# Kernel optimization log

Hardware: AMD Instinct MI355X
Metric: run time of the kernel (lower is better)

The kernel has to match this reference:

```python
import jax, jax.numpy as jnp
import numpy as np

N, E = 50000, 800000
IN_C, OUT_C, HEADS = 128, 16, 8
EDGE_DIM = 1
NEG_SLOPE = 0.2
LN_EPS = 1e-5


def setup_inputs() -> dict:
    key = jax.random.key(0)
    ks = jax.random.split(key, 12)
    s = 1.0 / np.sqrt(IN_C)
    HC = OUT_C * HEADS
    return {
        "x": jax.random.normal(ks[0], (N, IN_C), jnp.float32),
        "edge_index": jax.random.randint(ks[1], (2, E), 0, N, jnp.int32),
        "edge_attr": jax.random.normal(ks[2], (E, EDGE_DIM), jnp.float32),
        "W": jax.random.normal(ks[3], (IN_C, HC), jnp.float32) * s,
        "b": jnp.zeros((HC,), jnp.float32),
        "att_src": jax.random.normal(ks[4], (HEADS, OUT_C), jnp.float32) * s,
        "att_dst": jax.random.normal(ks[5], (HEADS, OUT_C), jnp.float32) * s,
        "att_edge": jax.random.normal(ks[6], (HEADS, OUT_C), jnp.float32) * s,
        "lin_edge_w": jax.random.normal(ks[7], (EDGE_DIM, HC), jnp.float32) * s,
        "lin_edge_b": jnp.zeros((HC,), jnp.float32),
        "gamma": jnp.ones((HC,), jnp.float32),
        "beta": jnp.zeros((HC,), jnp.float32),
    }


def _segment_softmax(logits, seg, num_segments):
    # numerically-stable softmax over edges grouped by destination node
    m = jax.ops.segment_max(logits, seg, num_segments=num_segments)
    ex = jnp.exp(logits - m[seg])
    z = jax.ops.segment_sum(ex, seg, num_segments=num_segments)
    return ex / (z[seg] + 1e-16)


def reference(x, edge_index, edge_attr, W, b, att_src, att_dst, att_edge,
              lin_edge_w, lin_edge_b, gamma, beta):
    n = x.shape[0]
    src, dst = edge_index[0], edge_index[1]
    # GAT conv: per-head transform, edge-indexed attention, segment softmax, scatter-add
    h = (x @ W).reshape(n, HEADS, OUT_C)                      # [N,H,C]
    a_src = jnp.einsum('nhc,hc->nh', h, att_src)              # [N,H]
    a_dst = jnp.einsum('nhc,hc->nh', h, att_dst)
    e = (edge_attr @ lin_edge_w + lin_edge_b).reshape(-1, HEADS, OUT_C)
    a_edge = jnp.einsum('ehc,hc->eh', e, att_edge)            # [E,H]
    logits = jax.nn.leaky_relu(a_src[src] + a_dst[dst] + a_edge, NEG_SLOPE)
    alpha = _segment_softmax(logits, dst, n)                  # [E,H]
    msg = alpha[..., None] * h[src]                           # [E,H,C]
    out = jax.ops.segment_sum(msg, dst, num_segments=n).reshape(n, -1) + b
    # residual (in_channels == heads*out_channels -> identity projection)
    out = out + x
    # LayerNorm + ELU (dropout is eval-mode identity)
    mu = jnp.mean(out, axis=-1, keepdims=True)
    var = jnp.var(out, axis=-1, keepdims=True)
    out = (out - mu) * jax.lax.rsqrt(var + LN_EPS) * gamma + beta
    return jax.nn.elu(out)
```

## Files before the change

kernel.cpp:

```cpp
#include <hip/hip_runtime.h>
#include <hip/hip_bf16.h>

#define N_NODES 50000
#define N_EDGES 800000
#define IN_C 128
#define HC 128
#define HEADS 8
#define NEG_SLOPE 0.2f
#define LN_EPS 1e-5f

#define LDH 136
#define ELL_CAP 64
#define FUSED_BLOCKS 1568
#define NBUCK 98
#define BCAP 26
#define ARENA_NCAP 9216
#define OVF_CAP 8192

typedef __hip_bfloat16 bf16;
typedef __attribute__((ext_vector_type(8))) short short8;
typedef __attribute__((ext_vector_type(4))) float f32x4;
typedef unsigned long long u64;

__device__ __forceinline__ float b2f(bf16 v) { return __bfloat162float(v); }

__device__ __forceinline__ unsigned short f2bf(float f) {
    unsigned u = __float_as_uint(f);
    return (unsigned short)((u + 0x7fffu + ((u >> 16) & 1u)) >> 16);
}
__device__ __forceinline__ float bf2f(unsigned s) {
    return __uint_as_float(s << 16);
}
__device__ __forceinline__ short8 pack8(float4 u, float4 v) {
    short8 r;
    r[0] = (short)f2bf(u.x); r[1] = (short)f2bf(u.y);
    r[2] = (short)f2bf(u.z); r[3] = (short)f2bf(u.w);
    r[4] = (short)f2bf(v.x); r[5] = (short)f2bf(v.y);
    r[6] = (short)f2bf(v.z); r[7] = (short)f2bf(v.w);
    return r;
}

__global__ __launch_bounds__(256) void prep(
    const float* __restrict__ W, unsigned short* __restrict__ Wt,
    int* __restrict__ actl)
{
    int id = blockIdx.x * 256 + threadIdx.x;
    int k = id >> 7, n = id & 127;
    Wt[n * 128 + k] = f2bf(W[id]);
    if (id < 128) actl[id] = 0;
}

__global__ __launch_bounds__(256) void fused(
    const float* __restrict__ x, const unsigned short* __restrict__ Wt,
    const float* __restrict__ att_src, const float* __restrict__ att_dst,
    const int* __restrict__ ei, const float* __restrict__ edge_attr,
    int* __restrict__ actl, u64* __restrict__ ovf, u64* __restrict__ arena,
    unsigned short* __restrict__ h_out,
    float* __restrict__ a_src, float* __restrict__ a_dst)
{
    __shared__ union {
        short sH[4][16 * LDH];
        struct {
            u64 recs[NBUCK][BCAP];
            int lcnt[NBUCK];
            int sbase[NBUCK];
        } bin;
    } sm;
    const int bid = blockIdx.x;
    const int t   = threadIdx.x;
    const int grp = bid >> 3;
    const int sub = bid & 7;

    if (grp & 1) {
        const int blk = (grp >> 1) * 8 + sub;
        if (t < NBUCK) sm.bin.lcnt[t] = 0;
        __syncthreads();

        const int e0 = blk * 1024 + t * 4;
        if (e0 < N_EDGES) {
            const int4   s4 = *reinterpret_cast<const int4*>(ei + e0);
            const int4   d4 = *reinterpret_cast<const int4*>(ei + N_EDGES + e0);
            const float4 a4 = *reinterpret_cast<const float4*>(edge_attr + e0);
#define BIN1(D, S, A)                                                      \
            {                                                              \
                const unsigned w_ =                                        \
                    (((unsigned)(S)) << 16) | (unsigned)f2bf(A);           \
                const int b_ = (D) >> 9;                                   \
                int p_ = atomicAdd(&sm.bin.lcnt[b_], 1);                   \
                if (p_ < BCAP)                                             \
                    sm.bin.recs[b_][p_] =                                  \
                        ((u64)(unsigned)((D) & 511) << 32) | (u64)w_;      \
                else {                                                     \
                    int op_ = atomicAdd(&actl[98], 1);                     \
                    if (op_ < OVF_CAP)                                     \
                        ovf[op_] = ((u64)(unsigned)(D) << 32) | (u64)w_;   \
                }                                                          \
            }
            BIN1(d4.x, s4.x, a4.x)
            BIN1(d4.y, s4.y, a4.y)
            BIN1(d4.z, s4.z, a4.z)
            BIN1(d4.w, s4.w, a4.w)
#undef BIN1
        }
        __syncthreads();
        if (t < NBUCK) {
            int k = min(sm.bin.lcnt[t], BCAP);
            sm.bin.sbase[t] = atomicAdd(&actl[t], k);
            sm.bin.lcnt[t]  = k;
        }
        __syncthreads();
        for (int i = t; i < NBUCK * BCAP; i += 256) {
            const int bi = i / BCAP;
            const int j  = i - bi * BCAP;
            if (j < sm.bin.lcnt[bi]) {
                const int pos = sm.bin.sbase[bi] + j;
                if (pos < ARENA_NCAP)
                    arena[(size_t)bi * ARENA_NCAP + pos] = sm.bin.recs[bi][j];
            }
        }
        return;
    }

    const int gid = (grp >> 1) * 8 + sub;
    const int wv  = t >> 6;
    const int l   = t & 63;
    const int gw  = gid * 4 + wv;
    if (gw >= N_NODES / 16) return;

    const int n0   = gw * 16;
    const int mrow = l & 15;
    const int quad = l >> 4;

    short8 afrag[4];
    const float* xr = x + (size_t)(n0 + mrow) * IN_C + quad * 8;
#pragma unroll
    for (int ko = 0; ko < 4; ++ko) {
        float4 u = *reinterpret_cast<const float4*>(xr + ko * 32);
        float4 v = *reinterpret_cast<const float4*>(xr + ko * 32 + 4);
        afrag[ko] = pack8(u, v);
    }

    f32x4 acc[8];
#pragma unroll
    for (int nt = 0; nt < 8; ++nt) acc[nt] = (f32x4)0.f;
#pragma unroll
    for (int nt = 0; nt < 8; ++nt) {
        const unsigned short* wr = Wt + (nt * 16 + mrow) * 128 + quad * 8;
#pragma unroll
        for (int ko = 0; ko < 4; ++ko) {
            short8 bfr = *reinterpret_cast<const short8*>(wr + ko * 32);
            acc[nt] = __builtin_amdgcn_mfma_f32_16x16x32_bf16(afrag[ko], bfr, acc[nt], 0, 0, 0);
        }
    }

#pragma unroll
    for (int nt = 0; nt < 8; ++nt)
#pragma unroll
        for (int r = 0; r < 4; ++r)
            sm.sH[wv][(quad * 4 + r) * LDH + nt * 16 + mrow] = (short)f2bf(acc[nt][r]);

#pragma unroll
    for (int i = 0; i < 4; ++i) {
        int row = i * 4 + (l >> 4);
        int col = (l & 15) * 8;
        short8 hv = *reinterpret_cast<const short8*>(&sm.sH[wv][row * LDH + col]);
        *reinterpret_cast<short8*>(h_out + (size_t)(n0 + row) * HC + col) = hv;
    }

#pragma unroll
    for (int pp = 0; pp < 2; ++pp) {
        int p  = l + pp * 64;
        int m  = p >> 3;
        int hd = p & 7;
        float ssum = 0.f, dsum = 0.f;
#pragma unroll
        for (int c = 0; c < 16; ++c) {
            float hv = bf2f((unsigned short)sm.sH[wv][m * LDH + hd * 16 + c]);
            ssum = fmaf(hv, att_src[hd * 16 + c], ssum);
            dsum = fmaf(hv, att_dst[hd * 16 + c], dsum);
        }
        a_src[(n0 + m) * HEADS + hd] = ssum;
        a_dst[(n0 + m) * HEADS + hd] = dsum;
    }
}

__global__ __launch_bounds__(1024) void ebuild(
    const u64* __restrict__ arena, const int* __restrict__ actl,
    const u64* __restrict__ ovf,
    unsigned int* __restrict__ ellp, int* __restrict__ cnt)
{
    __shared__ int lc[512];
    const int t = threadIdx.x;
    const int b = blockIdx.x;
    if (t < 512) lc[t] = 0;
    __syncthreads();

    const int nE = min(actl[b], ARENA_NCAP);
    const u64* seg = arena + (size_t)b * ARENA_NCAP;
    for (int q = t; q < nE; q += 1024) {
        const u64 rec = seg[q];
        const int dl = (int)(rec >> 32);
        int p = atomicAdd(&lc[dl], 1);
        if (p < ELL_CAP)
            ellp[((size_t)((b << 9) + dl) << 6) + p] = (unsigned)rec;
    }
    const int ovn = min(actl[98], OVF_CAP);
    for (int q = t; q < ovn; q += 1024) {
        const u64 rec = ovf[q];
        const int n = (int)(rec >> 32);
        if ((n >> 9) == b) {
            int p = atomicAdd(&lc[n & 511], 1);
            if (p < ELL_CAP)
                ellp[((size_t)n << 6) + p] = (unsigned)rec;
        }
    }
    __syncthreads();
    if (t < 512) {
        const int n = (b << 9) + t;
        if (n < N_NODES) cnt[n] = min(lc[t], ELL_CAP);
    }
}


#define LROW(CE, HV, J, OFF, B0)                                           \
    { int cj_ = __builtin_amdgcn_ds_swizzle((int)(CE), OFF);               \
      size_t r_ = ((B0) + (J) < cn) ? (size_t)(((unsigned)cj_) >> 16) : 0; \
      (HV)[J] = h2[r_ * 64 + l]; }
#define LOADROWS(CE, HV, B0)                                               \
    LROW(CE, HV, 0,  24, B0) LROW(CE, HV, 1,  56, B0)                      \
    LROW(CE, HV, 2,  88, B0) LROW(CE, HV, 3, 120, B0)                      \
    LROW(CE, HV, 4, 152, B0) LROW(CE, HV, 5, 184, B0)                      \
    LROW(CE, HV, 6, 216, B0) LROW(CE, HV, 7, 248, B0)

#define FROW(EV, HV, J, OFF)                                               \
    { float evj_ = __uint_as_float((unsigned)__builtin_amdgcn_ds_swizzle(  \
          __float_as_int(EV), OFF));                                       \
      acc0 = fmaf(evj_, b2f((HV)[J].x), acc0);                             \
      acc1 = fmaf(evj_, b2f((HV)[J].y), acc1); }
#define FMAROWS(EV, HV)                                                    \
    FROW(EV, HV, 0,  24) FROW(EV, HV, 1,  56) FROW(EV, HV, 2,  88)        \
    FROW(EV, HV, 3, 120) FROW(EV, HV, 4, 152) FROW(EV, HV, 5, 184)        \
    FROW(EV, HV, 6, 216) FROW(EV, HV, 7, 248)

__global__ __launch_bounds__(256) void gather_node(
    const int* __restrict__ cnt, const unsigned int* __restrict__ ellp,
    const float* __restrict__ a_src, const float* __restrict__ a_dst,
    const bf16* __restrict__ h,
    const float* __restrict__ x, const float* __restrict__ bvec,
    const float* __restrict__ gamma, const float* __restrict__ beta,
    const float* __restrict__ att_edge, const float* __restrict__ lin_w,
    const float* __restrict__ lin_b,
    float* __restrict__ out)
{
    const int wave = threadIdx.x >> 6;
    const int l    = threadIdx.x & 63;
    const int n    = blockIdx.x * 4 + wave;
    const int hh   = l >> 3;
    const int jj   = l & 7;

    float ae0 = att_edge[2 * l], ae1 = att_edge[2 * l + 1];
    float p = ae0 * lin_w[2 * l] + ae1 * lin_w[2 * l + 1];
    float q = ae0 * lin_b[2 * l] + ae1 * lin_b[2 * l + 1];
#pragma unroll
    for (int off = 1; off <= 4; off <<= 1) {
        p += __shfl_xor(p, off, 64);
        q += __shfl_xor(q, off, 64);
    }
    const float2 bv = *reinterpret_cast<const float2*>(bvec + 2 * l);
    const float2 gv = *reinterpret_cast<const float2*>(gamma + 2 * l);
    const float2 be = *reinterpret_cast<const float2*>(beta + 2 * l);

    const float adq = a_dst[n * HEADS + hh] + q;
    const int   beg = n << 6;
    const int   cn  = min(cnt[n], ELL_CAP);

    float zp = 0.f, acc0 = 0.f, acc1 = 0.f;
    const __hip_bfloat162* h2 = reinterpret_cast<const __hip_bfloat162*>(h);

    if (cn > 0) {
        unsigned ce_c = ellp[beg + jj];
        float    as_c = a_src[(ce_c >> 16) * HEADS + hh];
        __hip_bfloat162 hv_c[8], hv_n[8];
        LOADROWS(ce_c, hv_c, 0)

        for (int bs = 0; ; bs += 8) {
            const unsigned ce   = ce_c;
            const float    as   = as_c;
            const bool     last = (bs + 8 >= cn);
            if (!last) {
                ce_c = ellp[beg + bs + 8 + jj];
                LOADROWS(ce_c, hv_n, bs + 8)
                as_c = a_src[(ce_c >> 16) * HEADS + hh];
            }
            const float ea = bf2f(ce & 0xffffu);
            float lg = fmaf(ea, p, as + adq);
            lg = fmaxf(lg, NEG_SLOPE * lg);
            const float ev = (bs + jj < cn) ? __expf(lg) : 0.f;
            zp += ev;
            FMAROWS(ev, hv_c)
            if (last) break;
#pragma unroll
            for (int j = 0; j < 8; ++j) hv_c[j] = hv_n[j];
        }
    }

    float z = zp;
    z += __shfl_xor(z, 1, 64);
    z += __shfl_xor(z, 2, 64);
    z += __shfl_xor(z, 4, 64);
    const float rz = 1.f / (z + 1e-16f);
    acc0 *= rz;
    acc1 *= rz;

    const size_t idx = (size_t)n * HC + 2 * l;
    const float2 xv = *reinterpret_cast<const float2*>(x + idx);
    float v0 = acc0 + xv.x + bv.x;
    float v1 = acc1 + xv.y + bv.y;
    float s1 = v0 + v1, s2 = v0 * v0 + v1 * v1;
#pragma unroll
    for (int off = 32; off >= 1; off >>= 1) {
        s1 += __shfl_xor(s1, off, 64);
        s2 += __shfl_xor(s2, off, 64);
    }
    const float mean = s1 * (1.f / HC);
    const float var  = s2 * (1.f / HC) - mean * mean;
    const float inv  = rsqrtf(var + LN_EPS);
    float y0 = (v0 - mean) * inv * gv.x + be.x;
    float y1 = (v1 - mean) * inv * gv.y + be.y;
    y0 = y0 > 0.f ? y0 : expm1f(y0);
    y1 = y1 > 0.f ? y1 : expm1f(y1);
    *reinterpret_cast<float2*>(out + idx) = make_float2(y0, y1);
}

extern "C" void kernel_launch(void* const* d_in, const int* in_sizes, int n_in,
                              void* d_out, int out_size, void* d_ws, size_t ws_size,
                              hipStream_t stream)
{
    const float* x         = (const float*)d_in[0];
    const int*   ei        = (const int*)d_in[1];
    const float* edge_attr = (const float*)d_in[2];
    const float* W         = (const float*)d_in[3];
    const float* b         = (const float*)d_in[4];
    const float* att_src   = (const float*)d_in[5];
    const float* att_dst   = (const float*)d_in[6];
    const float* att_edge  = (const float*)d_in[7];
    const float* lin_w     = (const float*)d_in[8];
    const float* lin_b     = (const float*)d_in[9];
    const float* gamma     = (const float*)d_in[10];
    const float* beta      = (const float*)d_in[11];

    char* ws = (char*)d_ws;
    bf16*  h     = (bf16*)ws;  ws += (size_t)N_NODES * HC * sizeof(bf16);
    float* a_src = (float*)ws; ws += (size_t)N_NODES * HEADS * sizeof(float);
    float* a_dst = (float*)ws; ws += (size_t)N_NODES * HEADS * sizeof(float);
    int*   cnt   = (int*)ws;   ws += (size_t)N_NODES * sizeof(int);
    unsigned short* Wt = (unsigned short*)ws;
    ws += (size_t)128 * 128 * sizeof(unsigned short);
    unsigned int* ellp = (unsigned int*)ws;
    ws += (size_t)(N_NODES * ELL_CAP + 64) * sizeof(unsigned int);
    int* actl = (int*)ws;      ws += 128 * sizeof(int);
    u64* ovf  = (u64*)ws;      ws += (size_t)OVF_CAP * sizeof(u64);
    u64* arena = (u64*)d_out;

    prep<<<64, 256, 0, stream>>>(W, Wt, actl);

    fused<<<FUSED_BLOCKS, 256, 0, stream>>>(
        x, Wt, att_src, att_dst, ei, edge_attr, actl, ovf, arena,
        (unsigned short*)h, a_src, a_dst);

    ebuild<<<NBUCK, 1024, 0, stream>>>(arena, actl, ovf, ellp, cnt);

    gather_node<<<N_NODES / 4, 256, 0, stream>>>(
        cnt, ellp, a_src, a_dst, h, x, b, gamma, beta,
        att_edge, lin_w, lin_b, (float*)d_out);
}
```

Measured before the change: 202.3 us.

## Replace global bucket atomics with fixed per-block arena slots and count table

```diff
diff --git a/kernel.cpp b/kernel.cpp
--- a/kernel.cpp
+++ b/kernel.cpp
@@ -11,11 +11,12 @@
 
 #define LDH 136
 #define ELL_CAP 64
-#define FUSED_BLOCKS 1568
+#define GEMM_BLOCKS 782
+#define FILL_BLOCKS 782
+#define FUSED_BLOCKS (GEMM_BLOCKS + FILL_BLOCKS)
 #define NBUCK 98
 #define BCAP 26
-#define ARENA_NCAP 9216
-#define OVF_CAP 8192
+#define OVF_CAP 4096
 
 typedef __hip_bfloat16 bf16;
 typedef __attribute__((ext_vector_type(8))) short short8;
@@ -40,39 +41,109 @@
     return r;
 }
 
+union FusedSm {
+    short sH[4][16 * LDH];
+    struct {
+        u64 recs[NBUCK][BCAP];
+        int lcnt[NBUCK];
+    } bin;
+};
+
 __global__ __launch_bounds__(256) void prep(
     const float* __restrict__ W, unsigned short* __restrict__ Wt,
-    int* __restrict__ actl)
+    int* __restrict__ ovfc)
 {
     int id = blockIdx.x * 256 + threadIdx.x;
     int k = id >> 7, n = id & 127;
     Wt[n * 128 + k] = f2bf(W[id]);
-    if (id < 128) actl[id] = 0;
+    if (id == 0) *ovfc = 0;
+}
+
+__device__ __forceinline__ void gemm_body(
+    int gid, int t,
+    const float* __restrict__ x, const unsigned short* __restrict__ Wt,
+    const float* __restrict__ att_src, const float* __restrict__ att_dst,
+    unsigned short* __restrict__ h_out,
+    float* __restrict__ a_src, float* __restrict__ a_dst,
+    short (*sH)[16 * LDH])
+{
+    const int wv  = t >> 6;
+    const int l   = t & 63;
+    const int gw  = gid * 4 + wv;
+    if (gw >= N_NODES / 16) return;
+
+    const int n0   = gw * 16;
+    const int mrow = l & 15;
+    const int quad = l >> 4;
+
+    short8 afrag[4];
+    const float* xr = x + (size_t)(n0 + mrow) * IN_C + quad * 8;
+#pragma unroll
+    for (int ko = 0; ko < 4; ++ko) {
+        float4 u = *reinterpret_cast<const float4*>(xr + ko * 32);
+        float4 v = *reinterpret_cast<const float4*>(xr + ko * 32 + 4);
+        afrag[ko] = pack8(u, v);
+    }
+
+    f32x4 acc[8];
+#pragma unroll
+    for (int nt = 0; nt < 8; ++nt) acc[nt] = (f32x4)0.f;
+#pragma unroll
+    for (int nt = 0; nt < 8; ++nt) {
+        const unsigned short* wr = Wt + (nt * 16 + mrow) * 128 + quad * 8;
+#pragma unroll
+        for (int ko = 0; ko < 4; ++ko) {
+            short8 bfr = *reinterpret_cast<const short8*>(wr + ko * 32);
+            acc[nt] = __builtin_amdgcn_mfma_f32_16x16x32_bf16(afrag[ko], bfr, acc[nt], 0, 0, 0);
+        }
+    }
+
+#pragma unroll
+    for (int nt = 0; nt < 8; ++nt)
+#pragma unroll
+        for (int r = 0; r < 4; ++r)
+            sH[wv][(quad * 4 + r) * LDH + nt * 16 + mrow] = (short)f2bf(acc[nt][r]);
+
+#pragma unroll
+    for (int i = 0; i < 4; ++i) {
+        int row = i * 4 + (l >> 4);
+        int col = (l & 15) * 8;
+        short8 hv = *reinterpret_cast<const short8*>(&sH[wv][row * LDH + col]);
+        *reinterpret_cast<short8*>(h_out + (size_t)(n0 + row) * HC + col) = hv;
+    }
+
+#pragma unroll
+    for (int pp = 0; pp < 2; ++pp) {
+        int p  = l + pp * 64;
+        int m  = p >> 3;
+        int hd = p & 7;
+        float ssum = 0.f, dsum = 0.f;
+#pragma unroll
+        for (int c = 0; c < 16; ++c) {
+            float hv = bf2f((unsigned short)sH[wv][m * LDH + hd * 16 + c]);
+            ssum = fmaf(hv, att_src[hd * 16 + c], ssum);
+            dsum = fmaf(hv, att_dst[hd * 16 + c], dsum);
+        }
+        a_src[(n0 + m) * HEADS + hd] = ssum;
+        a_dst[(n0 + m) * HEADS + hd] = dsum;
+    }
 }
 
 __global__ __launch_bounds__(256) void fused(
     const float* __restrict__ x, const unsigned short* __restrict__ Wt,
     const float* __restrict__ att_src, const float* __restrict__ att_dst,
     const int* __restrict__ ei, const float* __restrict__ edge_attr,
-    int* __restrict__ actl, u64* __restrict__ ovf, u64* __restrict__ arena,
+    u64* __restrict__ arena, unsigned short* __restrict__ bcnt,
+    int* __restrict__ ovfc, u64* __restrict__ ovf,
     unsigned short* __restrict__ h_out,
     float* __restrict__ a_src, float* __restrict__ a_dst)
 {
-    __shared__ union {
-        short sH[4][16 * LDH];
-        struct {
-            u64 recs[NBUCK][BCAP];
-            int lcnt[NBUCK];
-            int sbase[NBUCK];
-        } bin;
-    } sm;
+    __shared__ FusedSm sm;
     const int bid = blockIdx.x;
     const int t   = threadIdx.x;
-    const int grp = bid >> 3;
-    const int sub = bid & 7;
-
-    if (grp & 1) {
-        const int blk = (grp >> 1) * 8 + sub;
+
+    if (bid & 1) {
+        const int blk = bid >> 1;
         if (t < NBUCK) sm.bin.lcnt[t] = 0;
         __syncthreads();
 
@@ -91,7 +162,7 @@
                     sm.bin.recs[b_][p_] =                                  \
                         ((u64)(unsigned)((D) & 511) << 32) | (u64)w_;      \
                 else {                                                     \
-                    int op_ = atomicAdd(&actl[98], 1);                     \
+                    int op_ = atomicAdd(ovfc, 1);                          \
                     if (op_ < OVF_CAP)                                     \
                         ovf[op_] = ((u64)(unsigned)(D) << 32) | (u64)w_;   \
                 }                                                          \
@@ -105,106 +176,49 @@
         __syncthreads();
         if (t < NBUCK) {
             int k = min(sm.bin.lcnt[t], BCAP);
-            sm.bin.sbase[t] = atomicAdd(&actl[t], k);
-            sm.bin.lcnt[t]  = k;
+            sm.bin.lcnt[t] = k;
+            bcnt[blk * NBUCK + t] = (unsigned short)k;
         }
         __syncthreads();
         for (int i = t; i < NBUCK * BCAP; i += 256) {
             const int bi = i / BCAP;
             const int j  = i - bi * BCAP;
-            if (j < sm.bin.lcnt[bi]) {
-                const int pos = sm.bin.sbase[bi] + j;
-                if (pos < ARENA_NCAP)
-                    arena[(size_t)bi * ARENA_NCAP + pos] = sm.bin.recs[bi][j];
-            }
+            if (j < sm.bin.lcnt[bi])
+                arena[((size_t)bi * FILL_BLOCKS + blk) * BCAP + j] =
+                    sm.bin.recs[bi][j];
         }
         return;
     }
 
-    const int gid = (grp >> 1) * 8 + sub;
-    const int wv  = t >> 6;
-    const int l   = t & 63;
-    const int gw  = gid * 4 + wv;
-    if (gw >= N_NODES / 16) return;
-
-    const int n0   = gw * 16;
-    const int mrow = l & 15;
-    const int quad = l >> 4;
-
-    short8 afrag[4];
-    const float* xr = x + (size_t)(n0 + mrow) * IN_C + quad * 8;
-#pragma unroll
-    for (int ko = 0; ko < 4; ++ko) {
-        float4 u = *reinterpret_cast<const float4*>(xr + ko * 32);
-        float4 v = *reinterpret_cast<const float4*>(xr + ko * 32 + 4);
-        afrag[ko] = pack8(u, v);
-    }
-
-    f32x4 acc[8];
-#pragma unroll
-    for (int nt = 0; nt < 8; ++nt) acc[nt] = (f32x4)0.f;
-#pragma unroll
-    for (int nt = 0; nt < 8; ++nt) {
-        const unsigned short* wr = Wt + (nt * 16 + mrow) * 128 + quad * 8;
-#pragma unroll
-        for (int ko = 0; ko < 4; ++ko) {
-            short8 bfr = *reinterpret_cast<const short8*>(wr + ko * 32);
-            acc[nt] = __builtin_amdgcn_mfma_f32_16x16x32_bf16(afrag[ko], bfr, acc[nt], 0, 0, 0);
-        }
-    }
-
-#pragma unroll
-    for (int nt = 0; nt < 8; ++nt)
-#pragma unroll
-        for (int r = 0; r < 4; ++r)
-            sm.sH[wv][(quad * 4 + r) * LDH + nt * 16 + mrow] = (short)f2bf(acc[nt][r]);
-
-#pragma unroll
-    for (int i = 0; i < 4; ++i) {
-        int row = i * 4 + (l >> 4);
-        int col = (l & 15) * 8;
-        short8 hv = *reinterpret_cast<const short8*>(&sm.sH[wv][row * LDH + col]);
-        *reinterpret_cast<short8*>(h_out + (size_t)(n0 + row) * HC + col) = hv;
-    }
-
-#pragma unroll
-    for (int pp = 0; pp < 2; ++pp) {
-        int p  = l + pp * 64;
-        int m  = p >> 3;
-        int hd = p & 7;
-        float ssum = 0.f, dsum = 0.f;
-#pragma unroll
-        for (int c = 0; c < 16; ++c) {
-            float hv = bf2f((unsigned short)sm.sH[wv][m * LDH + hd * 16 + c]);
-            ssum = fmaf(hv, att_src[hd * 16 + c], ssum);
-            dsum = fmaf(hv, att_dst[hd * 16 + c], dsum);
-        }
-        a_src[(n0 + m) * HEADS + hd] = ssum;
-        a_dst[(n0 + m) * HEADS + hd] = dsum;
-    }
+    gemm_body(bid >> 1, t, x, Wt, att_src, att_dst, h_out, a_src, a_dst, sm.sH);
 }
 
 __global__ __launch_bounds__(1024) void ebuild(
-    const u64* __restrict__ arena, const int* __restrict__ actl,
-    const u64* __restrict__ ovf,
+    const u64* __restrict__ arena, const unsigned short* __restrict__ bcnt,
+    const int* __restrict__ ovfc, const u64* __restrict__ ovf,
     unsigned int* __restrict__ ellp, int* __restrict__ cnt)
 {
     __shared__ int lc[512];
+    __shared__ unsigned short sbc[FILL_BLOCKS];
     const int t = threadIdx.x;
     const int b = blockIdx.x;
     if (t < 512) lc[t] = 0;
+    if (t < FILL_BLOCKS) sbc[t] = bcnt[t * NBUCK + b];
     __syncthreads();
 
-    const int nE = min(actl[b], ARENA_NCAP);
-    const u64* seg = arena + (size_t)b * ARENA_NCAP;
-    for (int q = t; q < nE; q += 1024) {
-        const u64 rec = seg[q];
-        const int dl = (int)(rec >> 32);
-        int p = atomicAdd(&lc[dl], 1);
-        if (p < ELL_CAP)
-            ellp[((size_t)((b << 9) + dl) << 6) + p] = (unsigned)rec;
-    }
-    const int ovn = min(actl[98], OVF_CAP);
+    const u64* seg = arena + (size_t)b * (FILL_BLOCKS * BCAP);
+    for (int q = t; q < FILL_BLOCKS * BCAP; q += 1024) {
+        const int blk = q / BCAP;
+        const int sl  = q - blk * BCAP;
+        if (sl < (int)sbc[blk]) {
+            const u64 rec = seg[q];
+            const int dl = (int)(rec >> 32);
+            int p = atomicAdd(&lc[dl], 1);
+            if (p < ELL_CAP)
+                ellp[((size_t)((b << 9) + dl) << 6) + p] = (unsigned)rec;
+        }
+    }
+    const int ovn = min(*ovfc, OVF_CAP);
     for (int q = t; q < ovn; q += 1024) {
         const u64 rec = ovf[q];
         const int n = (int)(rec >> 32);
@@ -358,17 +372,19 @@
     ws += (size_t)128 * 128 * sizeof(unsigned short);
     unsigned int* ellp = (unsigned int*)ws;
     ws += (size_t)(N_NODES * ELL_CAP + 64) * sizeof(unsigned int);
-    int* actl = (int*)ws;      ws += 128 * sizeof(int);
+    unsigned short* bcnt = (unsigned short*)ws;
+    ws += (size_t)FILL_BLOCKS * NBUCK * sizeof(unsigned short);
+    int* ovfc = (int*)ws;      ws += 64;
     u64* ovf  = (u64*)ws;      ws += (size_t)OVF_CAP * sizeof(u64);
     u64* arena = (u64*)d_out;
 
-    prep<<<64, 256, 0, stream>>>(W, Wt, actl);
+    prep<<<64, 256, 0, stream>>>(W, Wt, ovfc);
 
     fused<<<FUSED_BLOCKS, 256, 0, stream>>>(
-        x, Wt, att_src, att_dst, ei, edge_attr, actl, ovf, arena,
+        x, Wt, att_src, att_dst, ei, edge_attr, arena, bcnt, ovfc, ovf,
         (unsigned short*)h, a_src, a_dst);
 
-    ebuild<<<NBUCK, 1024, 0, stream>>>(arena, actl, ovf, ellp, cnt);
+    ebuild<<<NBUCK, 1024, 0, stream>>>(arena, bcnt, ovfc, ovf, ellp, cnt);
 
     gather_node<<<N_NODES / 4, 256, 0, stream>>>(
         cnt, ellp, a_src, a_dst, h, x, b, gamma, beta,
```

Result: faster. 191.5 us (-5.3%).
